# Kernel optimization log

Hardware: AMD Instinct MI355X
Metric: run time of the kernel (lower is better)

The kernel has to match this reference:

```python
import jax, jax.numpy as jnp
import numpy as np
from jax import lax

# module config (matches init_kwargs)
IN_CHANNELS = 1
NUM_OR = 8               # 360 / angle_res(45)
THRESHOLD = 0.9
WINDOW = (5, 5)
STRIDE = (1, 1)
WINDOW_SCALE = float(WINDOW[0] * WINDOW[1])
NORMALIZE_COUNT = True   # normalize_count=True -> avg counts (avg_pool2d semantics)


def setup_inputs() -> dict:
    key = jax.random.key(0)
    k1, k2 = jax.random.split(key)
    x = jax.random.normal(k1, (16, IN_CHANNELS, 1024, 1024), dtype=jnp.float32)
    # edge-orientation masks (Sobel rotations in the original; values are fixed
    # buffers, so random stand-ins preserve the exact compute pattern)
    masks = jax.random.normal(k2, (IN_CHANNELS * NUM_OR, 1, 3, 3), dtype=jnp.float32)
    return {"x": x, "masks": masks}


def reference(x, masks):
    # grouped edge-filter conv: [B,C,H,W] x [C*O,1,3,3] -> [B,C*O,H-2,W-2]
    y = lax.conv_general_dilated(
        x, masks, window_strides=(1, 1), padding='VALID',
        rhs_dilation=(1, 1), feature_group_count=IN_CHANNELS,
        dimension_numbers=('NCHW', 'OIHW', 'NCHW'))
    value = jnp.max(y, axis=1)    # [B,H',W']
    index = jnp.argmax(y, axis=1)  # dominant orientation per pixel
    # below-threshold responses assigned to the extra 'no edge' bin
    index = jnp.where(value < THRESHOLD, NUM_OR, index)
    # one-hot over NUM_OR+1 bins -> [B, NUM_OR+1, H', W']
    bins = (index[:, None, :, :] ==
            jnp.arange(NUM_OR + 1)[None, :, None, None]).astype(jnp.float32)
    # windowed histogram counts (avg_pool2d with no padding => plain window mean)
    counts = lax.reduce_window(bins, 0.0, lax.add,
                               (1, 1) + WINDOW, (1, 1) + STRIDE, 'VALID')
    feat = counts / WINDOW_SCALE if NORMALIZE_COUNT else counts
    return feat  # [B, NUM_OR+1, H'-4, W'-4]
```

## Files before the change

kernel.cpp:

```cpp
#include <hip/hip_runtime.h>


#define NOR 8
#define HH  1024
#define WW  1024
#define H2  1018
#define W2  1018
#define RPB 16
#define NIT (RPB + 4)

__global__ __launch_bounds__(256, 4)
void ehd_rows(const float* __restrict__ x,
              const float* __restrict__ masks,
              float* __restrict__ out)
{
    __shared__ unsigned long long oh[2][WW];

    const int t  = threadIdx.x;
    const int j0 = t * 4;
    const int r0 = blockIdx.x * RPB;
    const int b  = blockIdx.y;
    const float* xb = x + (long)b * HH * WW;

    float m[NOR][9];
#pragma unroll
    for (int o = 0; o < NOR; ++o)
#pragma unroll
        for (int k = 0; k < 9; ++k)
            m[o][k] = masks[o * 9 + k];

    const int jc = (j0 + 4 > WW - 2) ? (WW - 2) : (j0 + 4);

    float wr[3][6];
#pragma unroll
    for (int s = 0; s < 3; ++s) {
        const float4 a  = *reinterpret_cast<const float4*>(xb + (r0 + s) * WW + j0);
        const float2 bb = *reinterpret_cast<const float2*>(xb + (r0 + s) * WW + jc);
        wr[s][0] = a.x; wr[s][1] = a.y; wr[s][2] = a.z; wr[s][3] = a.w;
        wr[s][4] = bb.x; wr[s][5] = bb.y;
    }

    unsigned long long hs[5][4];
#pragma unroll
    for (int q = 0; q < 5; ++q)
#pragma unroll
        for (int c = 0; c < 4; ++c) hs[q][c] = 0ull;

    for (int rr = 0; rr < NIT; ++rr) {
        int nr = r0 + rr + 3; if (nr > HH - 1) nr = HH - 1;
        const float4 pa = *reinterpret_cast<const float4*>(xb + nr * WW + j0);
        const float2 pb = *reinterpret_cast<const float2*>(xb + nr * WW + jc);

        unsigned long long* ohc = oh[rr & 1];

        unsigned long long ohv[4];
#pragma unroll
        for (int c = 0; c < 4; ++c) {
            float best = 0.0f; int bi = 0;
#pragma unroll
            for (int o = 0; o < NOR; ++o) {
                float acc = wr[0][c] * m[o][0];
                acc = fmaf(wr[0][c + 1], m[o][1], acc);
                acc = fmaf(wr[0][c + 2], m[o][2], acc);
                acc = fmaf(wr[1][c    ], m[o][3], acc);
                acc = fmaf(wr[1][c + 1], m[o][4], acc);
                acc = fmaf(wr[1][c + 2], m[o][5], acc);
                acc = fmaf(wr[2][c    ], m[o][6], acc);
                acc = fmaf(wr[2][c + 1], m[o][7], acc);
                acc = fmaf(wr[2][c + 2], m[o][8], acc);
                if (o == 0)          { best = acc; }
                else if (acc > best) { best = acc; bi = o; }
            }
            if (best < 0.9f) bi = NOR;
            ohv[c] = 1ull << (7 * bi);
        }
        if (t < 255) {
#pragma unroll
            for (int c = 0; c < 4; ++c) ohc[j0 + c] = ohv[c];
        } else {
            ohc[j0]     = ohv[0];
            ohc[j0 + 1] = ohv[1];
        }
        __syncthreads();

        if (t < 255) {
            const unsigned long long o4 = ohc[j0 + 4];
            const unsigned long long o5 = ohc[j0 + 5];
            const unsigned long long o6 = ohc[j0 + 6];
            const unsigned long long o7 = ohc[j0 + 7];
            const unsigned long long s0 = ohv[0] + ohv[1] + ohv[2] + ohv[3] + o4;
            const unsigned long long s1 = s0 + o5 - ohv[0];
            const unsigned long long s2 = s1 + o6 - ohv[1];
            const unsigned long long s3 = s2 + o7 - ohv[2];

#pragma unroll
            for (int q = 0; q < 4; ++q)
#pragma unroll
                for (int c = 0; c < 4; ++c) hs[q][c] = hs[q + 1][c];
            hs[4][0] = s0; hs[4][1] = s1; hs[4][2] = s2; hs[4][3] = s3;

            if (rr >= 4) {
                const int ro = r0 + rr - 4;
                if (ro < H2) {
                    const unsigned long long v0 = hs[0][0] + hs[1][0] + hs[2][0] + hs[3][0] + hs[4][0];
                    const unsigned long long v1 = hs[0][1] + hs[1][1] + hs[2][1] + hs[3][1] + hs[4][1];
                    const unsigned long long v2 = hs[0][2] + hs[1][2] + hs[2][2] + hs[3][2] + hs[4][2];
                    const unsigned long long v3 = hs[0][3] + hs[1][3] + hs[2][3] + hs[3][3] + hs[4][3];
                    float* op = out + ((long)b * 9 * H2 + (long)ro) * W2 + j0;
                    if (t < 254) {
#pragma unroll
                        for (int k = 0; k < 9; ++k) {
                            const float f0 = (float)((unsigned)(v0 >> (7 * k)) & 0x7Fu) * (1.0f / 25.0f);
                            const float f1 = (float)((unsigned)(v1 >> (7 * k)) & 0x7Fu) * (1.0f / 25.0f);
                            const float f2 = (float)((unsigned)(v2 >> (7 * k)) & 0x7Fu) * (1.0f / 25.0f);
                            const float f3 = (float)((unsigned)(v3 >> (7 * k)) & 0x7Fu) * (1.0f / 25.0f);
                            float2* q2 = reinterpret_cast<float2*>(op + (long)k * H2 * W2);
                            q2[0] = make_float2(f0, f1);
                            q2[1] = make_float2(f2, f3);
                        }
                    } else {
#pragma unroll
                        for (int k = 0; k < 9; ++k) {
                            const float f0 = (float)((unsigned)(v0 >> (7 * k)) & 0x7Fu) * (1.0f / 25.0f);
                            const float f1 = (float)((unsigned)(v1 >> (7 * k)) & 0x7Fu) * (1.0f / 25.0f);
                            float* q1 = op + (long)k * H2 * W2;
                            q1[0] = f0;
                            q1[1] = f1;
                        }
                    }
                }
            }
        }

#pragma unroll
        for (int d = 0; d < 6; ++d) {
            wr[0][d] = wr[1][d];
            wr[1][d] = wr[2][d];
        }
        wr[2][0] = pa.x; wr[2][1] = pa.y; wr[2][2] = pa.z; wr[2][3] = pa.w;
        wr[2][4] = pb.x; wr[2][5] = pb.y;
    }
}

extern "C" void kernel_launch(void* const* d_in, const int* in_sizes, int n_in,
                              void* d_out, int out_size, void* d_ws, size_t ws_size,
                              hipStream_t stream)
{
    const float* x     = (const float*)d_in[0];
    const float* masks = (const float*)d_in[1];
    float* out         = (float*)d_out;

    dim3 grid((H2 + RPB - 1) / RPB,
              16);
    ehd_rows<<<grid, 256, 0, stream>>>(x, masks, out);
}
```

Measured before the change: 698.1 us.

## Replace shared-memory one-hot exchange and barrier with wavefront shuffles

The horizontal 5-wide window sum used to read neighbouring lanes' one-hot codes from a double-buffered shared array, which needed a __syncthreads every row. Now each lane builds prefix sums of its four codes and takes its neighbour's prefixes with a 64-bit shuffle-down. Lanes on a wavefront boundary recompute the neighbour's four pixels themselves from extra halo loads. This drops the shared memory and the per-row block barrier, at the cost of redundant convolution work and divergence on one lane per wavefront.

```diff
diff --git a/kernel.cpp b/kernel.cpp
--- a/kernel.cpp
+++ b/kernel.cpp
@@ -9,13 +9,20 @@
 #define RPB 16
 #define NIT (RPB + 4)
 
+__device__ __forceinline__ unsigned long long shfl_down_u64(unsigned long long v)
+{
+    unsigned int lo = (unsigned int)(v & 0xFFFFFFFFull);
+    unsigned int hi = (unsigned int)(v >> 32);
+    lo = __shfl_down(lo, 1);
+    hi = __shfl_down(hi, 1);
+    return ((unsigned long long)hi << 32) | (unsigned long long)lo;
+}
+
 __global__ __launch_bounds__(256, 4)
 void ehd_rows(const float* __restrict__ x,
               const float* __restrict__ masks,
               float* __restrict__ out)
 {
-    __shared__ unsigned long long oh[2][WW];
-
     const int t  = threadIdx.x;
     const int j0 = t * 4;
     const int r0 = blockIdx.x * RPB;
@@ -30,14 +37,22 @@
             m[o][k] = masks[o * 9 + k];
 
     const int jc = (j0 + 4 > WW - 2) ? (WW - 2) : (j0 + 4);
+    const bool bnd = ((t & 63) == 63) && (t != 255);
 
     float wr[3][6];
+    float wh[3][4];
 #pragma unroll
     for (int s = 0; s < 3; ++s) {
         const float4 a  = *reinterpret_cast<const float4*>(xb + (r0 + s) * WW + j0);
         const float2 bb = *reinterpret_cast<const float2*>(xb + (r0 + s) * WW + jc);
         wr[s][0] = a.x; wr[s][1] = a.y; wr[s][2] = a.z; wr[s][3] = a.w;
         wr[s][4] = bb.x; wr[s][5] = bb.y;
+        wh[s][0] = 0.f; wh[s][1] = 0.f; wh[s][2] = 0.f; wh[s][3] = 0.f;
+        if (bnd) {
+            const float2 h0 = *reinterpret_cast<const float2*>(xb + (r0 + s) * WW + j0 + 6);
+            const float2 h1 = *reinterpret_cast<const float2*>(xb + (r0 + s) * WW + j0 + 8);
+            wh[s][0] = h0.x; wh[s][1] = h0.y; wh[s][2] = h1.x; wh[s][3] = h1.y;
+        }
     }
 
     unsigned long long hs[5][4];
@@ -50,8 +65,12 @@
         int nr = r0 + rr + 3; if (nr > HH - 1) nr = HH - 1;
         const float4 pa = *reinterpret_cast<const float4*>(xb + nr * WW + j0);
         const float2 pb = *reinterpret_cast<const float2*>(xb + nr * WW + jc);
-
-        unsigned long long* ohc = oh[rr & 1];
+        float ph[4] = {0.f, 0.f, 0.f, 0.f};
+        if (bnd) {
+            const float2 h0 = *reinterpret_cast<const float2*>(xb + nr * WW + j0 + 6);
+            const float2 h1 = *reinterpret_cast<const float2*>(xb + nr * WW + j0 + 8);
+            ph[0] = h0.x; ph[1] = h0.y; ph[2] = h1.x; ph[3] = h1.y;
+        }
 
         unsigned long long ohv[4];
 #pragma unroll
@@ -74,59 +93,84 @@
             if (best < 0.9f) bi = NOR;
             ohv[c] = 1ull << (7 * bi);
         }
-        if (t < 255) {
-#pragma unroll
-            for (int c = 0; c < 4; ++c) ohc[j0 + c] = ohv[c];
-        } else {
-            ohc[j0]     = ohv[0];
-            ohc[j0 + 1] = ohv[1];
-        }
-        __syncthreads();
-
-        if (t < 255) {
-            const unsigned long long o4 = ohc[j0 + 4];
-            const unsigned long long o5 = ohc[j0 + 5];
-            const unsigned long long o6 = ohc[j0 + 6];
-            const unsigned long long o7 = ohc[j0 + 7];
-            const unsigned long long s0 = ohv[0] + ohv[1] + ohv[2] + ohv[3] + o4;
-            const unsigned long long s1 = s0 + o5 - ohv[0];
-            const unsigned long long s2 = s1 + o6 - ohv[1];
-            const unsigned long long s3 = s2 + o7 - ohv[2];
-
-#pragma unroll
-            for (int q = 0; q < 4; ++q)
-#pragma unroll
-                for (int c = 0; c < 4; ++c) hs[q][c] = hs[q + 1][c];
-            hs[4][0] = s0; hs[4][1] = s1; hs[4][2] = s2; hs[4][3] = s3;
-
-            if (rr >= 4) {
-                const int ro = r0 + rr - 4;
-                if (ro < H2) {
-                    const unsigned long long v0 = hs[0][0] + hs[1][0] + hs[2][0] + hs[3][0] + hs[4][0];
-                    const unsigned long long v1 = hs[0][1] + hs[1][1] + hs[2][1] + hs[3][1] + hs[4][1];
-                    const unsigned long long v2 = hs[0][2] + hs[1][2] + hs[2][2] + hs[3][2] + hs[4][2];
-                    const unsigned long long v3 = hs[0][3] + hs[1][3] + hs[2][3] + hs[3][3] + hs[4][3];
-                    float* op = out + ((long)b * 9 * H2 + (long)ro) * W2 + j0;
-                    if (t < 254) {
-#pragma unroll
-                        for (int k = 0; k < 9; ++k) {
-                            const float f0 = (float)((unsigned)(v0 >> (7 * k)) & 0x7Fu) * (1.0f / 25.0f);
-                            const float f1 = (float)((unsigned)(v1 >> (7 * k)) & 0x7Fu) * (1.0f / 25.0f);
-                            const float f2 = (float)((unsigned)(v2 >> (7 * k)) & 0x7Fu) * (1.0f / 25.0f);
-                            const float f3 = (float)((unsigned)(v3 >> (7 * k)) & 0x7Fu) * (1.0f / 25.0f);
-                            float2* q2 = reinterpret_cast<float2*>(op + (long)k * H2 * W2);
-                            q2[0] = make_float2(f0, f1);
-                            q2[1] = make_float2(f2, f3);
-                        }
-                    } else {
-#pragma unroll
-                        for (int k = 0; k < 9; ++k) {
-                            const float f0 = (float)((unsigned)(v0 >> (7 * k)) & 0x7Fu) * (1.0f / 25.0f);
-                            const float f1 = (float)((unsigned)(v1 >> (7 * k)) & 0x7Fu) * (1.0f / 25.0f);
-                            float* q1 = op + (long)k * H2 * W2;
-                            q1[0] = f0;
-                            q1[1] = f1;
-                        }
+
+        unsigned long long hp1 = 0, hp2 = 0, hp3 = 0, hp4 = 0;
+        if (bnd) {
+            const float xh0[6] = { wr[0][4], wr[0][5], wh[0][0], wh[0][1], wh[0][2], wh[0][3] };
+            const float xh1[6] = { wr[1][4], wr[1][5], wh[1][0], wh[1][1], wh[1][2], wh[1][3] };
+            const float xh2[6] = { wr[2][4], wr[2][5], wh[2][0], wh[2][1], wh[2][2], wh[2][3] };
+            unsigned long long hv[4];
+#pragma unroll
+            for (int c = 0; c < 4; ++c) {
+                float best = 0.0f; int bi = 0;
+#pragma unroll
+                for (int o = 0; o < NOR; ++o) {
+                    float acc = xh0[c] * m[o][0];
+                    acc = fmaf(xh0[c + 1], m[o][1], acc);
+                    acc = fmaf(xh0[c + 2], m[o][2], acc);
+                    acc = fmaf(xh1[c    ], m[o][3], acc);
+                    acc = fmaf(xh1[c + 1], m[o][4], acc);
+                    acc = fmaf(xh1[c + 2], m[o][5], acc);
+                    acc = fmaf(xh2[c    ], m[o][6], acc);
+                    acc = fmaf(xh2[c + 1], m[o][7], acc);
+                    acc = fmaf(xh2[c + 2], m[o][8], acc);
+                    if (o == 0)          { best = acc; }
+                    else if (acc > best) { best = acc; bi = o; }
+                }
+                if (best < 0.9f) bi = NOR;
+                hv[c] = 1ull << (7 * bi);
+            }
+            hp1 = hv[0]; hp2 = hp1 + hv[1]; hp3 = hp2 + hv[2]; hp4 = hp3 + hv[3];
+        }
+
+        const unsigned long long p1 = ohv[0];
+        const unsigned long long p2 = p1 + ohv[1];
+        const unsigned long long p3 = p2 + ohv[2];
+        const unsigned long long p4 = p3 + ohv[3];
+        unsigned long long q1 = shfl_down_u64(p1);
+        unsigned long long q2 = shfl_down_u64(p2);
+        unsigned long long q3 = shfl_down_u64(p3);
+        unsigned long long q4 = shfl_down_u64(p4);
+        if (bnd) { q1 = hp1; q2 = hp2; q3 = hp3; q4 = hp4; }
+
+        const unsigned long long s0 = p4 + q1;
+        const unsigned long long s1 = (p4 - p1) + q2;
+        const unsigned long long s2 = (p4 - p2) + q3;
+        const unsigned long long s3 = ohv[3] + q4;
+
+#pragma unroll
+        for (int q = 0; q < 4; ++q)
+#pragma unroll
+            for (int c = 0; c < 4; ++c) hs[q][c] = hs[q + 1][c];
+        hs[4][0] = s0; hs[4][1] = s1; hs[4][2] = s2; hs[4][3] = s3;
+
+        if (rr >= 4) {
+            const int ro = r0 + rr - 4;
+            if (ro < H2 && t < 255) {
+                const unsigned long long v0 = hs[0][0] + hs[1][0] + hs[2][0] + hs[3][0] + hs[4][0];
+                const unsigned long long v1 = hs[0][1] + hs[1][1] + hs[2][1] + hs[3][1] + hs[4][1];
+                const unsigned long long v2 = hs[0][2] + hs[1][2] + hs[2][2] + hs[3][2] + hs[4][2];
+                const unsigned long long v3 = hs[0][3] + hs[1][3] + hs[2][3] + hs[3][3] + hs[4][3];
+                float* op = out + ((long)b * 9 * H2 + (long)ro) * W2 + j0;
+                if (t < 254) {
+#pragma unroll
+                    for (int k = 0; k < 9; ++k) {
+                        const float f0 = (float)((unsigned)(v0 >> (7 * k)) & 0x7Fu) * (1.0f / 25.0f);
+                        const float f1 = (float)((unsigned)(v1 >> (7 * k)) & 0x7Fu) * (1.0f / 25.0f);
+                        const float f2 = (float)((unsigned)(v2 >> (7 * k)) & 0x7Fu) * (1.0f / 25.0f);
+                        const float f3 = (float)((unsigned)(v3 >> (7 * k)) & 0x7Fu) * (1.0f / 25.0f);
+                        float2* q2s = reinterpret_cast<float2*>(op + (long)k * H2 * W2);
+                        q2s[0] = make_float2(f0, f1);
+                        q2s[1] = make_float2(f2, f3);
+                    }
+                } else {
+#pragma unroll
+                    for (int k = 0; k < 9; ++k) {
+                        const float f0 = (float)((unsigned)(v0 >> (7 * k)) & 0x7Fu) * (1.0f / 25.0f);
+                        const float f1 = (float)((unsigned)(v1 >> (7 * k)) & 0x7Fu) * (1.0f / 25.0f);
+                        float* q1s = op + (long)k * H2 * W2;
+                        q1s[0] = f0;
+                        q1s[1] = f1;
                     }
                 }
             }
@@ -139,6 +183,14 @@
         }
         wr[2][0] = pa.x; wr[2][1] = pa.y; wr[2][2] = pa.z; wr[2][3] = pa.w;
         wr[2][4] = pb.x; wr[2][5] = pb.y;
+        if (bnd) {
+#pragma unroll
+            for (int c = 0; c < 4; ++c) {
+                wh[0][c] = wh[1][c];
+                wh[1][c] = wh[2][c];
+                wh[2][c] = ph[c];
+            }
+        }
     }
 }
 
```

After: 764.7 us. 9.5% more time.

## Use taller row strips and 2-column threads with 512-thread blocks

Applied to the files above, without the earlier changes.

Each block now covers a 64-row strip instead of 16 rows, which cuts the 4-row vertical halo recomputation overhead. Each of 512 threads now handles 2 columns instead of 4, using vectorized shared-memory reads and writes of 64-bit histogram words. The grid shrinks to 16x16 blocks. That is one block per CU on a 256-CU part, so fewer waves are in flight to hide memory latency, and each block runs a longer serial loop with a barrier per row.

```diff
diff --git a/kernel.cpp b/kernel.cpp
--- a/kernel.cpp
+++ b/kernel.cpp
@@ -6,19 +6,19 @@
 #define WW  1024
 #define H2  1018
 #define W2  1018
-#define RPB 16
-#define NIT (RPB + 4)
+#define SH  64
+#define NIT (SH + 4)
 
-__global__ __launch_bounds__(256, 4)
+__global__ __launch_bounds__(512, 2)
 void ehd_rows(const float* __restrict__ x,
               const float* __restrict__ masks,
               float* __restrict__ out)
 {
-    __shared__ unsigned long long oh[2][WW];
+    __shared__ unsigned long long oh[2][1024];
 
     const int t  = threadIdx.x;
-    const int j0 = t * 4;
-    const int r0 = blockIdx.x * RPB;
+    const int j0 = t * 2;
+    const int r0 = blockIdx.x * SH;
     const int b  = blockIdx.y;
     const float* xb = x + (long)b * HH * WW;
 
@@ -29,116 +29,87 @@
         for (int k = 0; k < 9; ++k)
             m[o][k] = masks[o * 9 + k];
 
-    const int jc = (j0 + 4 > WW - 2) ? (WW - 2) : (j0 + 4);
+    const bool cvalid = (j0 <= 1020);
+    const bool ovalid = (j0 <= W2 - 2);
 
-    float wr[3][6];
+    const int jb = (j0 + 2 > WW - 2) ? (WW - 2) : (j0 + 2);
+
+    float wr[3][4];
 #pragma unroll
     for (int s = 0; s < 3; ++s) {
-        const float4 a  = *reinterpret_cast<const float4*>(xb + (r0 + s) * WW + j0);
-        const float2 bb = *reinterpret_cast<const float2*>(xb + (r0 + s) * WW + jc);
-        wr[s][0] = a.x; wr[s][1] = a.y; wr[s][2] = a.z; wr[s][3] = a.w;
-        wr[s][4] = bb.x; wr[s][5] = bb.y;
+        const float2 A = *reinterpret_cast<const float2*>(xb + (r0 + s) * WW + j0);
+        const float2 B = *reinterpret_cast<const float2*>(xb + (r0 + s) * WW + jb);
+        wr[s][0] = A.x; wr[s][1] = A.y; wr[s][2] = B.x; wr[s][3] = B.y;
     }
 
-    unsigned long long hs[5][4];
+    unsigned long long hs[5][2];
 #pragma unroll
-    for (int q = 0; q < 5; ++q)
-#pragma unroll
-        for (int c = 0; c < 4; ++c) hs[q][c] = 0ull;
+    for (int q = 0; q < 5; ++q) { hs[q][0] = 0ull; hs[q][1] = 0ull; }
 
     for (int rr = 0; rr < NIT; ++rr) {
         int nr = r0 + rr + 3; if (nr > HH - 1) nr = HH - 1;
-        const float4 pa = *reinterpret_cast<const float4*>(xb + nr * WW + j0);
-        const float2 pb = *reinterpret_cast<const float2*>(xb + nr * WW + jc);
+        const float2 pa = *reinterpret_cast<const float2*>(xb + nr * WW + j0);
+        const float2 pb = *reinterpret_cast<const float2*>(xb + nr * WW + jb);
 
-        unsigned long long* ohc = oh[rr & 1];
+        unsigned long long* ohb = oh[rr & 1];
 
-        unsigned long long ohv[4];
+        if (cvalid) {
+            unsigned long long ov[2];
 #pragma unroll
-        for (int c = 0; c < 4; ++c) {
-            float best = 0.0f; int bi = 0;
+            for (int c = 0; c < 2; ++c) {
+                float best = 0.0f; int bi = 0;
 #pragma unroll
-            for (int o = 0; o < NOR; ++o) {
-                float acc = wr[0][c] * m[o][0];
-                acc = fmaf(wr[0][c + 1], m[o][1], acc);
-                acc = fmaf(wr[0][c + 2], m[o][2], acc);
-                acc = fmaf(wr[1][c    ], m[o][3], acc);
-                acc = fmaf(wr[1][c + 1], m[o][4], acc);
-                acc = fmaf(wr[1][c + 2], m[o][5], acc);
-                acc = fmaf(wr[2][c    ], m[o][6], acc);
-                acc = fmaf(wr[2][c + 1], m[o][7], acc);
-                acc = fmaf(wr[2][c + 2], m[o][8], acc);
-                if (o == 0)          { best = acc; }
-                else if (acc > best) { best = acc; bi = o; }
+                for (int o = 0; o < NOR; ++o) {
+                    float acc = wr[0][c] * m[o][0];
+                    acc = fmaf(wr[0][c + 1], m[o][1], acc);
+                    acc = fmaf(wr[0][c + 2], m[o][2], acc);
+                    acc = fmaf(wr[1][c    ], m[o][3], acc);
+                    acc = fmaf(wr[1][c + 1], m[o][4], acc);
+                    acc = fmaf(wr[1][c + 2], m[o][5], acc);
+                    acc = fmaf(wr[2][c    ], m[o][6], acc);
+                    acc = fmaf(wr[2][c + 1], m[o][7], acc);
+                    acc = fmaf(wr[2][c + 2], m[o][8], acc);
+                    if (o == 0)          { best = acc; }
+                    else if (acc > best) { best = acc; bi = o; }
+                }
+                if (best < 0.9f) bi = NOR;
+                ov[c] = 1ull << (7 * bi);
             }
-            if (best < 0.9f) bi = NOR;
-            ohv[c] = 1ull << (7 * bi);
-        }
-        if (t < 255) {
-#pragma unroll
-            for (int c = 0; c < 4; ++c) ohc[j0 + c] = ohv[c];
-        } else {
-            ohc[j0]     = ohv[0];
-            ohc[j0 + 1] = ohv[1];
+            ulonglong2 wv; wv.x = ov[0]; wv.y = ov[1];
+            *reinterpret_cast<ulonglong2*>(&ohb[j0]) = wv;
         }
         __syncthreads();
 
-        if (t < 255) {
-            const unsigned long long o4 = ohc[j0 + 4];
-            const unsigned long long o5 = ohc[j0 + 5];
-            const unsigned long long o6 = ohc[j0 + 6];
-            const unsigned long long o7 = ohc[j0 + 7];
-            const unsigned long long s0 = ohv[0] + ohv[1] + ohv[2] + ohv[3] + o4;
-            const unsigned long long s1 = s0 + o5 - ohv[0];
-            const unsigned long long s2 = s1 + o6 - ohv[1];
-            const unsigned long long s3 = s2 + o7 - ohv[2];
+        if (ovalid) {
+            const ulonglong2 A  = *reinterpret_cast<const ulonglong2*>(&ohb[j0]);
+            const ulonglong2 Bv = *reinterpret_cast<const ulonglong2*>(&ohb[j0 + 2]);
+            const ulonglong2 Cv = *reinterpret_cast<const ulonglong2*>(&ohb[j0 + 4]);
+            const unsigned long long s0 = A.x + A.y + Bv.x + Bv.y + Cv.x;
+            const unsigned long long s1 = s0 - A.x + Cv.y;
 
 #pragma unroll
-            for (int q = 0; q < 4; ++q)
-#pragma unroll
-                for (int c = 0; c < 4; ++c) hs[q][c] = hs[q + 1][c];
-            hs[4][0] = s0; hs[4][1] = s1; hs[4][2] = s2; hs[4][3] = s3;
+            for (int q = 0; q < 4; ++q) { hs[q][0] = hs[q + 1][0]; hs[q][1] = hs[q + 1][1]; }
+            hs[4][0] = s0; hs[4][1] = s1;
 
             if (rr >= 4) {
                 const int ro = r0 + rr - 4;
                 if (ro < H2) {
                     const unsigned long long v0 = hs[0][0] + hs[1][0] + hs[2][0] + hs[3][0] + hs[4][0];
                     const unsigned long long v1 = hs[0][1] + hs[1][1] + hs[2][1] + hs[3][1] + hs[4][1];
-                    const unsigned long long v2 = hs[0][2] + hs[1][2] + hs[2][2] + hs[3][2] + hs[4][2];
-                    const unsigned long long v3 = hs[0][3] + hs[1][3] + hs[2][3] + hs[3][3] + hs[4][3];
-                    float* op = out + ((long)b * 9 * H2 + (long)ro) * W2 + j0;
-                    if (t < 254) {
+                    float* op = out + (long)b * 9 * H2 * W2 + (long)ro * W2 + j0;
 #pragma unroll
-                        for (int k = 0; k < 9; ++k) {
-                            const float f0 = (float)((unsigned)(v0 >> (7 * k)) & 0x7Fu) * (1.0f / 25.0f);
-                            const float f1 = (float)((unsigned)(v1 >> (7 * k)) & 0x7Fu) * (1.0f / 25.0f);
-                            const float f2 = (float)((unsigned)(v2 >> (7 * k)) & 0x7Fu) * (1.0f / 25.0f);
-                            const float f3 = (float)((unsigned)(v3 >> (7 * k)) & 0x7Fu) * (1.0f / 25.0f);
-                            float2* q2 = reinterpret_cast<float2*>(op + (long)k * H2 * W2);
-                            q2[0] = make_float2(f0, f1);
-                            q2[1] = make_float2(f2, f3);
-                        }
-                    } else {
-#pragma unroll
-                        for (int k = 0; k < 9; ++k) {
-                            const float f0 = (float)((unsigned)(v0 >> (7 * k)) & 0x7Fu) * (1.0f / 25.0f);
-                            const float f1 = (float)((unsigned)(v1 >> (7 * k)) & 0x7Fu) * (1.0f / 25.0f);
-                            float* q1 = op + (long)k * H2 * W2;
-                            q1[0] = f0;
-                            q1[1] = f1;
-                        }
+                    for (int k = 0; k < 9; ++k) {
+                        const float f0 = (float)((unsigned)(v0 >> (7 * k)) & 0x7Fu) * (1.0f / 25.0f);
+                        const float f1 = (float)((unsigned)(v1 >> (7 * k)) & 0x7Fu) * (1.0f / 25.0f);
+                        *reinterpret_cast<float2*>(op + (long)k * H2 * W2) = make_float2(f0, f1);
                     }
                 }
             }
         }
 
 #pragma unroll
-        for (int d = 0; d < 6; ++d) {
-            wr[0][d] = wr[1][d];
-            wr[1][d] = wr[2][d];
-        }
-        wr[2][0] = pa.x; wr[2][1] = pa.y; wr[2][2] = pa.z; wr[2][3] = pa.w;
-        wr[2][4] = pb.x; wr[2][5] = pb.y;
+        for (int d = 0; d < 4; ++d) { wr[0][d] = wr[1][d]; wr[1][d] = wr[2][d]; }
+        wr[2][0] = pa.x; wr[2][1] = pa.y; wr[2][2] = pb.x; wr[2][3] = pb.y;
     }
 }
 
@@ -150,7 +121,7 @@
     const float* masks = (const float*)d_in[1];
     float* out         = (float*)d_out;
 
-    dim3 grid((H2 + RPB - 1) / RPB,
+    dim3 grid(16,
               16);
-    ehd_rows<<<grid, 256, 0, stream>>>(x, masks, out);
+    ehd_rows<<<grid, 512, 0, stream>>>(x, masks, out);
 }
```

Measured after the change: 654.2 us, median of 2. 1.07x faster.
